# Kernel optimization log

Hardware: AMD Instinct MI355X
Metric: run time of the kernel (lower is better)

## Reference

```python
import jax, jax.numpy as jnp
import numpy as np

N, E, HDIM, NG = 10000, 320000, 256, 20
BN_EPS = 1e-5


def setup_inputs() -> dict:
    key = jax.random.key(0)
    ks = jax.random.split(key, 12)
    inp = {
        "x": jax.random.normal(ks[0], (N, HDIM), dtype=jnp.float32),
        "rbf": jax.random.uniform(ks[1], (E, NG), dtype=jnp.float32),
        "ei": jax.random.randint(ks[2], (2, E), 0, N, dtype=jnp.int64),
        # filter_net: Linear(n_g, hdim) -> SiLU -> Linear(hdim, hdim)
        "Wf1": jax.random.normal(ks[3], (NG, HDIM), dtype=jnp.float32) / np.sqrt(NG),
        "bf1": jnp.zeros((HDIM,), dtype=jnp.float32),
        "Wf2": jax.random.normal(ks[4], (HDIM, HDIM), dtype=jnp.float32) / np.sqrt(HDIM),
        "bf2": jnp.zeros((HDIM,), dtype=jnp.float32),
        # node_update: Linear(hdim, hdim) -> SiLU -> Linear(hdim, hdim)
        "Wu1": jax.random.normal(ks[5], (HDIM, HDIM), dtype=jnp.float32) / np.sqrt(HDIM),
        "bu1": jnp.zeros((HDIM,), dtype=jnp.float32),
        "Wu2": jax.random.normal(ks[6], (HDIM, HDIM), dtype=jnp.float32) / np.sqrt(HDIM),
        "bu2": jnp.zeros((HDIM,), dtype=jnp.float32),
        # BatchNorm1d affine params
        "gamma": jnp.ones((HDIM,), dtype=jnp.float32),
        "beta": jnp.zeros((HDIM,), dtype=jnp.float32),
    }
    return inp


def reference(x, rbf, Wf1, bf1, Wf2, bf2, Wu1, bu1, Wu2, bu2, gamma, beta, ei):
    row, col = ei[0], ei[1]
    # filter_net(rbf): [E, hdim]
    filt = jax.nn.silu(rbf @ Wf1 + bf1) @ Wf2 + bf2
    # message = gather(x, col) * filter
    msg = x[col] * filt  # [E, hdim]
    # scatter_add aggregation over destination nodes
    agg = jax.ops.segment_sum(msg, row, num_segments=x.shape[0])  # [N, hdim]
    # node_update MLP
    h = jax.nn.silu(agg @ Wu1 + bu1) @ Wu2 + bu2  # [N, hdim]
    # BatchNorm1d (training mode: batch stats, biased variance)
    mean = jnp.mean(h, axis=0)
    var = jnp.mean(jnp.square(h - mean), axis=0)
    bn = gamma * (h - mean) * jax.lax.rsqrt(var + BN_EPS) + beta
    return x + bn
```

## Files before the change

kernel.cpp:

```cpp
#include <hip/hip_runtime.h>

#define N_NODES 10000
#define E_EDGES 320000
#define HDIM    256
#define NG      20
#define BN_EPS  1e-5f

typedef __attribute__((ext_vector_type(8))) short short8;
typedef __attribute__((ext_vector_type(4))) float f32x4;

__device__ __forceinline__ float silu_f(float v) { return v / (1.0f + __expf(-v)); }

__device__ __forceinline__ unsigned short f2bf(float f) {
    union { float f; unsigned int u; } v; v.f = f;
    unsigned int r = v.u + 0x7fffu + ((v.u >> 16) & 1u);
    return (unsigned short)(r >> 16);
}

__global__ __launch_bounds__(256) void prep_kernel(
    const float* __restrict__ Wf2, const float* __restrict__ Wu1,
    const float* __restrict__ Wu2,
    unsigned short* __restrict__ Pf2, unsigned short* __restrict__ Pu1,
    unsigned short* __restrict__ Pu2)
{
    const float* W = (blockIdx.y == 0) ? Wf2 : (blockIdx.y == 1) ? Wu1 : Wu2;
    unsigned short* P = (blockIdx.y == 0) ? Pf2 : (blockIdx.y == 1) ? Pu1 : Pu2;
    int tid   = blockIdx.x * 256 + threadIdx.x;
    int j     = tid & 7;
    int lane  = (tid >> 3) & 63;
    int ntile = (tid >> 9) & 15;
    int kstep = tid >> 13;
    int k = kstep * 32 + (lane >> 4) * 8 + j;
    int n = ntile * 16 + (lane & 15);
    P[tid] = f2bf(W[k * 256 + n]);
}

__global__ __launch_bounds__(256) void prep1_kernel(
    const float* __restrict__ Wf1, const float* __restrict__ bf1,
    unsigned short* __restrict__ P1)
{
    int tid = blockIdx.x * 256 + threadIdx.x;
    int j     = tid & 7;
    int lane  = (tid >> 3) & 63;
    int ntile = tid >> 9;
    int k = (lane >> 4) * 8 + j;
    int n = ntile * 16 + (lane & 15);
    float v = (k < NG) ? Wf1[k * 256 + n] : (k == NG ? bf1[n] : 0.0f);
    P1[tid] = f2bf(v);
}

__global__ __launch_bounds__(256) void hist_kernel(const int* __restrict__ ei_row,
                                                   int* __restrict__ cnt) {
    int e = blockIdx.x * 256 + threadIdx.x;
    atomicAdd(&cnt[ei_row[e]], 1);
}

__global__ __launch_bounds__(256) void scan_kernel(int* __restrict__ cnt) {
    __shared__ int tot[256];
    const int t = threadIdx.x;
    int loc[40];
    int s = 0;
    #pragma unroll
    for (int i = 0; i < 40; ++i) { loc[i] = cnt[t * 40 + i]; s += loc[i]; }
    tot[t] = s;
    __syncthreads();
    for (int off = 1; off < 256; off <<= 1) {
        int u = (t >= off) ? tot[t - off] : 0;
        __syncthreads();
        tot[t] += u;
        __syncthreads();
    }
    int pre = tot[t] - s;
    #pragma unroll
    for (int i = 0; i < 40; ++i) { int v = loc[i]; cnt[t * 40 + i] = pre; pre += v; }
}

__global__ __launch_bounds__(256) void fill_kernel(const int* __restrict__ ei_row,
                                                   int* __restrict__ cnt,
                                                   int* __restrict__ perm,
                                                   int* __restrict__ nodepos) {
    int e = blockIdx.x * 256 + threadIdx.x;
    int r = ei_row[e];
    int pos = atomicAdd(&cnt[r], 1);
    perm[pos] = e;
    nodepos[pos] = r;
}

#define SM_A1  0
#define SM_NID 5120
#define SM_COL 5376
#define SM_HID 5632
#define SM_TOT 38400

__global__ __launch_bounds__(256, 3) void edge_kernel(
    const float* __restrict__ rbf, const int* __restrict__ ei_col,
    const int* __restrict__ perm, const int* __restrict__ nodepos,
    const unsigned short* __restrict__ P1, const unsigned short* __restrict__ P2,
    const float* __restrict__ bf2, const float* __restrict__ x,
    float* __restrict__ agg)
{
    __shared__ char sm[SM_TOT];
    unsigned short* A1 = (unsigned short*)(sm + SM_A1);
    int* nid_s = (int*)(sm + SM_NID);
    int* col_s = (int*)(sm + SM_COL);

    const int t  = threadIdx.x;
    const int p0 = blockIdx.x * 64;
    const int l = t & 63, w = t >> 6;
    const int l15 = l & 15, l4 = l >> 4;

    if (t < 64) {
        nid_s[t] = nodepos[p0 + t];
        col_s[t] = ei_col[perm[p0 + t]];
    }
    {
        const int row = t >> 2, q = t & 3;
        const int e = perm[p0 + row];
        const float* rp = rbf + (size_t)e * NG + q * 5;
        #pragma unroll
        for (int i = 0; i < 5; ++i) A1[row * 40 + q * 5 + i] = f2bf(rp[i]);
        if (q == 3) {
            A1[row * 40 + 20] = 0x3F80;
            #pragma unroll
            for (int k = 21; k < 32; ++k) A1[row * 40 + k] = 0;
        }
    }

    short8 b1[4];
    #pragma unroll
    for (int n = 0; n < 4; ++n)
        b1[n] = *(const short8*)(P1 + ((4 * w + n) * 64 + l) * 8);

    __syncthreads();

    f32x4 acc[4][4];
    #pragma unroll
    for (int n = 0; n < 4; ++n)
        #pragma unroll
        for (int m = 0; m < 4; ++m) acc[n][m] = (f32x4)0.0f;

    #pragma unroll
    for (int m = 0; m < 4; ++m) {
        short8 af = *(const short8*)(sm + SM_A1 + (m * 16 + l15) * 80 + l4 * 16);
        #pragma unroll
        for (int n = 0; n < 4; ++n)
            acc[n][m] = __builtin_amdgcn_mfma_f32_16x16x32_bf16(af, b1[n], acc[n][m], 0, 0, 0);
    }

    #pragma unroll
    for (int n = 0; n < 4; ++n) {
        const int col = w * 64 + n * 16 + l15;
        #pragma unroll
        for (int m = 0; m < 4; ++m)
            #pragma unroll
            for (int r = 0; r < 4; ++r) {
                int row = m * 16 + l4 * 4 + r;
                *(unsigned short*)(sm + SM_HID + row * 512 +
                    ((((col >> 3) ^ (row & 7))) << 4) + (col & 7) * 2) =
                    f2bf(silu_f(acc[n][m][r]));
            }
    }
    __syncthreads();

    #pragma unroll
    for (int n = 0; n < 4; ++n)
        #pragma unroll
        for (int m = 0; m < 4; ++m) acc[n][m] = (f32x4)0.0f;

    short8 bcur[4];
    #pragma unroll
    for (int n = 0; n < 4; ++n)
        bcur[n] = *(const short8*)(P2 + (((0 * 16 + 4 * w + n) * 64) + l) * 8);

    for (int ks = 0; ks < 8; ++ks) {
        short8 bnext[4];
        if (ks < 7) {
            #pragma unroll
            for (int n = 0; n < 4; ++n)
                bnext[n] = *(const short8*)(P2 + ((((ks + 1) * 16 + 4 * w + n) * 64) + l) * 8);
        }
        #pragma unroll
        for (int m = 0; m < 4; ++m) {
            const int row = m * 16 + l15;
            short8 af = *(const short8*)(sm + SM_HID + row * 512 +
                           ((((ks << 2) + l4) ^ (row & 7)) << 4));
            #pragma unroll
            for (int n = 0; n < 4; ++n)
                acc[n][m] = __builtin_amdgcn_mfma_f32_16x16x32_bf16(af, bcur[n], acc[n][m], 0, 0, 0);
        }
        if (ks < 7) {
            #pragma unroll
            for (int n = 0; n < 4; ++n) bcur[n] = bnext[n];
        }
    }
    __syncthreads();

    float bc[4];
    #pragma unroll
    for (int n = 0; n < 4; ++n) bc[n] = bf2[w * 64 + n * 16 + l15];

    float sum = 0.0f;
    int cur = nid_s[0];
    float* msgf = (float*)(sm + SM_HID);

    #pragma unroll
    for (int ms = 0; ms < 2; ++ms) {
        #pragma unroll
        for (int mm = 0; mm < 2; ++mm) {
            const int m = ms * 2 + mm;
            #pragma unroll
            for (int r = 0; r < 4; ++r) {
                const int row = m * 16 + l4 * 4 + r;
                const int pos = row & 31;
                const float* xp = x + (size_t)col_s[row] * HDIM;
                #pragma unroll
                for (int n = 0; n < 4; ++n) {
                    const int col = w * 64 + n * 16 + l15;
                    float mv = (acc[n][m][r] + bc[n]) * xp[col];
                    *(float*)(sm + SM_HID + pos * 1024 +
                        ((((col >> 2) ^ (pos & 7))) << 4) + (col & 3) * 4) = mv;
                }
            }
        }
        __syncthreads();
        for (int pos = 0; pos < 32; ++pos) {
            const int row = ms * 32 + pos;
            const int nid = nid_s[row];
            float v = *(const float*)(sm + SM_HID + pos * 1024 +
                        ((((t >> 2) ^ (pos & 7))) << 4) + (t & 3) * 4);
            if (nid != cur) {
                atomicAdd(&agg[(size_t)cur * HDIM + t], sum);
                sum = 0.0f; cur = nid;
            }
            sum += v;
        }
        __syncthreads();
    }
    atomicAdd(&agg[(size_t)cur * HDIM + t], sum);
}

__global__ __launch_bounds__(256, 3) void node_kernel(
    const float* __restrict__ agg, const float* __restrict__ bu1,
    const float* __restrict__ bu2,
    const unsigned short* __restrict__ Pu1, const unsigned short* __restrict__ Pu2,
    float* __restrict__ hout, float* __restrict__ sums)
{
    __shared__ unsigned short A[64 * 256];
    const int t  = threadIdx.x;
    const int r0 = blockIdx.x * 64;
    const int l = t & 63, w = t >> 6;
    const int l15 = l & 15, l4 = l >> 4;

    {
        const int kq = t >> 3, klo = t & 7;
        for (int row = 0; row < 64; ++row) {
            int gr = r0 + row;
            float v = (gr < N_NODES) ? agg[(size_t)gr * HDIM + t] : 0.0f;
            A[row * 256 + ((kq ^ (row & 7)) << 3) + klo] = f2bf(v);
        }
    }
    __syncthreads();

    f32x4 acc[4][4];
    #pragma unroll
    for (int n = 0; n < 4; ++n)
        #pragma unroll
        for (int m = 0; m < 4; ++m) acc[n][m] = (f32x4)0.0f;

    short8 bcur[4];
    #pragma unroll
    for (int n = 0; n < 4; ++n)
        bcur[n] = *(const short8*)(Pu1 + (((4 * w + n) * 64) + l) * 8);

    for (int ks = 0; ks < 8; ++ks) {
        short8 bnext[4];
        if (ks < 7) {
            #pragma unroll
            for (int n = 0; n < 4; ++n)
                bnext[n] = *(const short8*)(Pu1 + ((((ks + 1) * 16 + 4 * w + n) * 64) + l) * 8);
        }
        #pragma unroll
        for (int m = 0; m < 4; ++m) {
            const int row = m * 16 + l15;
            short8 af = *(const short8*)((char*)A + row * 512 +
                           ((((ks << 2) + l4) ^ (row & 7)) << 4));
            #pragma unroll
            for (int n = 0; n < 4; ++n)
                acc[n][m] = __builtin_amdgcn_mfma_f32_16x16x32_bf16(af, bcur[n], acc[n][m], 0, 0, 0);
        }
        if (ks < 7) {
            #pragma unroll
            for (int n = 0; n < 4; ++n) bcur[n] = bnext[n];
        }
    }
    __syncthreads();

    #pragma unroll
    for (int n = 0; n < 4; ++n) {
        const int col = w * 64 + n * 16 + l15;
        const float b = bu1[col];
        #pragma unroll
        for (int m = 0; m < 4; ++m)
            #pragma unroll
            for (int r = 0; r < 4; ++r) {
                int row = m * 16 + l4 * 4 + r;
                A[row * 256 + (((col >> 3) ^ (row & 7)) << 3) + (col & 7)] =
                    f2bf(silu_f(acc[n][m][r] + b));
            }
    }
    #pragma unroll
    for (int n = 0; n < 4; ++n)
        #pragma unroll
        for (int m = 0; m < 4; ++m) acc[n][m] = (f32x4)0.0f;
    __syncthreads();

    #pragma unroll
    for (int n = 0; n < 4; ++n)
        bcur[n] = *(const short8*)(Pu2 + (((4 * w + n) * 64) + l) * 8);

    for (int ks = 0; ks < 8; ++ks) {
        short8 bnext[4];
        if (ks < 7) {
            #pragma unroll
            for (int n = 0; n < 4; ++n)
                bnext[n] = *(const short8*)(Pu2 + ((((ks + 1) * 16 + 4 * w + n) * 64) + l) * 8);
        }
        #pragma unroll
        for (int m = 0; m < 4; ++m) {
            const int row = m * 16 + l15;
            short8 af = *(const short8*)((char*)A + row * 512 +
                           ((((ks << 2) + l4) ^ (row & 7)) << 4));
            #pragma unroll
            for (int n = 0; n < 4; ++n)
                acc[n][m] = __builtin_amdgcn_mfma_f32_16x16x32_bf16(af, bcur[n], acc[n][m], 0, 0, 0);
        }
        if (ks < 7) {
            #pragma unroll
            for (int n = 0; n < 4; ++n) bcur[n] = bnext[n];
        }
    }

    #pragma unroll
    for (int n = 0; n < 4; ++n) {
        const int col = w * 64 + n * 16 + l15;
        const float b = bu2[col];
        float s = 0.0f, s2 = 0.0f;
        #pragma unroll
        for (int m = 0; m < 4; ++m)
            #pragma unroll
            for (int r = 0; r < 4; ++r) {
                int gr = r0 + m * 16 + l4 * 4 + r;
                float h = acc[n][m][r] + b;
                if (gr < N_NODES) {
                    hout[(size_t)gr * HDIM + col] = h;
                    s += h; s2 += h * h;
                }
            }
        s  += __shfl_xor(s, 16);  s  += __shfl_xor(s, 32);
        s2 += __shfl_xor(s2, 16); s2 += __shfl_xor(s2, 32);
        if (l4 == 0) {
            atomicAdd(&sums[col], s);
            atomicAdd(&sums[HDIM + col], s2);
        }
    }
}

__global__ __launch_bounds__(256) void final_kernel(
    const float* __restrict__ x, const float* __restrict__ sums,
    const float* __restrict__ gamma, const float* __restrict__ beta,
    float* __restrict__ out)
{
    const int i = blockIdx.x * 256 + threadIdx.x;
    const int j = i & (HDIM - 1);
    const float mean = sums[j] * (1.0f / N_NODES);
    const float var  = sums[HDIM + j] * (1.0f / N_NODES) - mean * mean;
    const float inv  = rsqrtf(var + BN_EPS);
    const float hv   = out[i];
    out[i] = x[i] + gamma[j] * (hv - mean) * inv + beta[j];
}

extern "C" void kernel_launch(void* const* d_in, const int* in_sizes, int n_in,
                              void* d_out, int out_size, void* d_ws, size_t ws_size,
                              hipStream_t stream) {
    const float* x     = (const float*)d_in[0];
    const float* rbf   = (const float*)d_in[1];
    const int*   ei    = (const int*)d_in[2];
    const float* Wf1   = (const float*)d_in[3];
    const float* bf1   = (const float*)d_in[4];
    const float* Wf2   = (const float*)d_in[5];
    const float* bf2   = (const float*)d_in[6];
    const float* Wu1   = (const float*)d_in[7];
    const float* bu1   = (const float*)d_in[8];
    const float* Wu2   = (const float*)d_in[9];
    const float* bu2   = (const float*)d_in[10];
    const float* gamma = (const float*)d_in[11];
    const float* beta  = (const float*)d_in[12];
    float* out = (float*)d_out;

    char* ws = (char*)d_ws;
    float* agg     = (float*)(ws);
    float* sums    = (float*)(ws + 10240000);
    int*   cnt     = (int*)(ws + 10242048);
    int*   perm    = (int*)(ws + 10283008);
    int*   nodepos = (int*)(ws + 11563008);
    unsigned short* Pf2 = (unsigned short*)(ws + 12843008);
    unsigned short* Pu1 = (unsigned short*)(ws + 12974080);
    unsigned short* Pu2 = (unsigned short*)(ws + 13105152);
    unsigned short* P1  = (unsigned short*)(ws + 13236224);

    hipMemsetAsync(agg,  0, 10240000, stream);
    hipMemsetAsync(sums, 0, 2048, stream);
    hipMemsetAsync(cnt,  0, 40960, stream);

    prep_kernel<<<dim3(256, 3), 256, 0, stream>>>(Wf2, Wu1, Wu2, Pf2, Pu1, Pu2);
    prep1_kernel<<<32, 256, 0, stream>>>(Wf1, bf1, P1);
    hist_kernel<<<E_EDGES / 256, 256, 0, stream>>>(ei, cnt);
    scan_kernel<<<1, 256, 0, stream>>>(cnt);
    fill_kernel<<<E_EDGES / 256, 256, 0, stream>>>(ei, cnt, perm, nodepos);

    edge_kernel<<<E_EDGES / 64, 256, 0, stream>>>(
        rbf, ei + E_EDGES, perm, nodepos, P1, Pf2, bf2, x, agg);
    node_kernel<<<(N_NODES + 63) / 64, 256, 0, stream>>>(
        agg, bu1, bu2, Pu1, Pu2, out, sums);
    final_kernel<<<(N_NODES * HDIM) / 256, 256, 0, stream>>>(x, sums, gamma, beta, out);
}
```

Measured before the change: 219.7 us.

## Transpose MFMA operand roles, vectorize epilogues, merge prep kernels and memsets

Swaps the MFMA operand roles so weights are the A operand and activations the B operand. Each lane then holds four consecutive output columns, which allows packed bf16 conversion and vectorized float4 loads and stores of x, bias, hout and the staged messages. It also merges the Wf1 prep into the main prep kernel, merges three memsets into one, vectorizes the rbf and agg staging loads, swizzles the edge block order across groups of eight, and uses a hardware reciprocal in SiLU. Together these cut launch count, scalar memory ops and conversion instructions. The cost is a more intricate fragment mapping and slightly less precise SiLU.

```diff
diff --git a/kernel.cpp b/kernel.cpp
--- a/kernel.cpp
+++ b/kernel.cpp
@@ -9,7 +9,16 @@
 typedef __attribute__((ext_vector_type(8))) short short8;
 typedef __attribute__((ext_vector_type(4))) float f32x4;
 
-__device__ __forceinline__ float silu_f(float v) { return v / (1.0f + __expf(-v)); }
+__device__ __forceinline__ float silu_f(float v) {
+    float e = __expf(-v);
+    return v * __builtin_amdgcn_rcpf(1.0f + e);
+}
+
+__device__ __forceinline__ unsigned int cvt_pk(float lo, float hi) {
+    unsigned int r;
+    asm("v_cvt_pk_bf16_f32 %0, %1, %2" : "=v"(r) : "v"(lo), "v"(hi));
+    return r;
+}
 
 __device__ __forceinline__ unsigned short f2bf(float f) {
     union { float f; unsigned int u; } v; v.f = f;
@@ -19,10 +28,23 @@
 
 __global__ __launch_bounds__(256) void prep_kernel(
     const float* __restrict__ Wf2, const float* __restrict__ Wu1,
-    const float* __restrict__ Wu2,
+    const float* __restrict__ Wu2, const float* __restrict__ Wf1,
+    const float* __restrict__ bf1,
     unsigned short* __restrict__ Pf2, unsigned short* __restrict__ Pu1,
-    unsigned short* __restrict__ Pu2)
+    unsigned short* __restrict__ Pu2, unsigned short* __restrict__ P1)
 {
+    if (blockIdx.y == 3) {
+        if (blockIdx.x >= 32) return;
+        int tid = blockIdx.x * 256 + threadIdx.x;
+        int j     = tid & 7;
+        int lane  = (tid >> 3) & 63;
+        int ntile = tid >> 9;
+        int k = (lane >> 4) * 8 + j;
+        int n = ntile * 16 + (lane & 15);
+        float v = (k < NG) ? Wf1[k * 256 + n] : (k == NG ? bf1[n] : 0.0f);
+        P1[tid] = f2bf(v);
+        return;
+    }
     const float* W = (blockIdx.y == 0) ? Wf2 : (blockIdx.y == 1) ? Wu1 : Wu2;
     unsigned short* P = (blockIdx.y == 0) ? Pf2 : (blockIdx.y == 1) ? Pu1 : Pu2;
     int tid   = blockIdx.x * 256 + threadIdx.x;
@@ -35,20 +57,6 @@
     P[tid] = f2bf(W[k * 256 + n]);
 }
 
-__global__ __launch_bounds__(256) void prep1_kernel(
-    const float* __restrict__ Wf1, const float* __restrict__ bf1,
-    unsigned short* __restrict__ P1)
-{
-    int tid = blockIdx.x * 256 + threadIdx.x;
-    int j     = tid & 7;
-    int lane  = (tid >> 3) & 63;
-    int ntile = tid >> 9;
-    int k = (lane >> 4) * 8 + j;
-    int n = ntile * 16 + (lane & 15);
-    float v = (k < NG) ? Wf1[k * 256 + n] : (k == NG ? bf1[n] : 0.0f);
-    P1[tid] = f2bf(v);
-}
-
 __global__ __launch_bounds__(256) void hist_kernel(const int* __restrict__ ei_row,
                                                    int* __restrict__ cnt) {
     int e = blockIdx.x * 256 + threadIdx.x;
@@ -86,11 +94,11 @@
     nodepos[pos] = r;
 }
 
-#define SM_A1  0
-#define SM_NID 5120
-#define SM_COL 5376
-#define SM_HID 5632
-#define SM_TOT 38400
+#define SM_NID 0
+#define SM_COL 256
+#define SM_RBF 512
+#define SM_HID 4608
+#define SM_TOT 37376
 
 __global__ __launch_bounds__(256, 3) void edge_kernel(
     const float* __restrict__ rbf, const int* __restrict__ ei_col,
@@ -100,12 +108,13 @@
     float* __restrict__ agg)
 {
     __shared__ char sm[SM_TOT];
-    unsigned short* A1 = (unsigned short*)(sm + SM_A1);
     int* nid_s = (int*)(sm + SM_NID);
     int* col_s = (int*)(sm + SM_COL);
 
-    const int t  = threadIdx.x;
-    const int p0 = blockIdx.x * 64;
+    const int t = threadIdx.x;
+    int blk = blockIdx.x;
+    blk = (blk & 7) * (E_EDGES / 64 / 8) + (blk >> 3);
+    const int p0 = blk * 64;
     const int l = t & 63, w = t >> 6;
     const int l15 = l & 15, l4 = l >> 4;
 
@@ -113,113 +122,122 @@
         nid_s[t] = nodepos[p0 + t];
         col_s[t] = ei_col[perm[p0 + t]];
     }
-    {
-        const int row = t >> 2, q = t & 3;
-        const int e = perm[p0 + row];
-        const float* rp = rbf + (size_t)e * NG + q * 5;
-        #pragma unroll
-        for (int i = 0; i < 5; ++i) A1[row * 40 + q * 5 + i] = f2bf(rp[i]);
-        if (q == 3) {
-            A1[row * 40 + 20] = 0x3F80;
-            #pragma unroll
-            for (int k = 21; k < 32; ++k) A1[row * 40 + k] = 0;
-        }
-    }
-
-    short8 b1[4];
-    #pragma unroll
-    for (int n = 0; n < 4; ++n)
-        b1[n] = *(const short8*)(P1 + ((4 * w + n) * 64 + l) * 8);
+    if (t < 128) {
+        const int row = t >> 1, half = t & 1;
+        const float* rp = rbf + (size_t)perm[p0 + row] * NG + half * 10;
+        float v[10];
+        if (half == 0) {
+            float4 a = *(const float4*)rp, b = *(const float4*)(rp + 4);
+            float2 c = *(const float2*)(rp + 8);
+            v[0]=a.x; v[1]=a.y; v[2]=a.z; v[3]=a.w; v[4]=b.x;
+            v[5]=b.y; v[6]=b.z; v[7]=b.w; v[8]=c.x; v[9]=c.y;
+        } else {
+            float2 a = *(const float2*)rp;
+            float4 b = *(const float4*)(rp + 2), c = *(const float4*)(rp + 6);
+            v[0]=a.x; v[1]=a.y; v[2]=b.x; v[3]=b.y; v[4]=b.z;
+            v[5]=b.w; v[6]=c.x; v[7]=c.y; v[8]=c.z; v[9]=c.w;
+        }
+        unsigned int* dst = (unsigned int*)(sm + SM_RBF + row * 64 + half * 20);
+        #pragma unroll
+        for (int i = 0; i < 5; ++i) dst[i] = cvt_pk(v[2*i], v[2*i+1]);
+    } else if (t < 192) {
+        const int row = t - 128;
+        *(unsigned long long*)(sm + SM_RBF + row * 64 + 40) = 0x3F80ull;
+        *(uint4*)(sm + SM_RBF + row * 64 + 48) = make_uint4(0, 0, 0, 0);
+    }
+
+    short8 a1[4], acur[4];
+    #pragma unroll
+    for (int mt = 0; mt < 4; ++mt) {
+        a1[mt]   = *(const short8*)(P1 + ((4 * w + mt) * 64 + l) * 8);
+        acur[mt] = *(const short8*)(P2 + ((4 * w + mt) * 64 + l) * 8);
+    }
 
     __syncthreads();
 
     f32x4 acc[4][4];
     #pragma unroll
-    for (int n = 0; n < 4; ++n)
-        #pragma unroll
-        for (int m = 0; m < 4; ++m) acc[n][m] = (f32x4)0.0f;
-
-    #pragma unroll
-    for (int m = 0; m < 4; ++m) {
-        short8 af = *(const short8*)(sm + SM_A1 + (m * 16 + l15) * 80 + l4 * 16);
-        #pragma unroll
-        for (int n = 0; n < 4; ++n)
-            acc[n][m] = __builtin_amdgcn_mfma_f32_16x16x32_bf16(af, b1[n], acc[n][m], 0, 0, 0);
-    }
-
-    #pragma unroll
-    for (int n = 0; n < 4; ++n) {
-        const int col = w * 64 + n * 16 + l15;
-        #pragma unroll
-        for (int m = 0; m < 4; ++m)
-            #pragma unroll
-            for (int r = 0; r < 4; ++r) {
-                int row = m * 16 + l4 * 4 + r;
-                *(unsigned short*)(sm + SM_HID + row * 512 +
-                    ((((col >> 3) ^ (row & 7))) << 4) + (col & 7) * 2) =
-                    f2bf(silu_f(acc[n][m][r]));
-            }
-    }
-    __syncthreads();
-
-    #pragma unroll
-    for (int n = 0; n < 4; ++n)
-        #pragma unroll
-        for (int m = 0; m < 4; ++m) acc[n][m] = (f32x4)0.0f;
-
-    short8 bcur[4];
-    #pragma unroll
-    for (int n = 0; n < 4; ++n)
-        bcur[n] = *(const short8*)(P2 + (((0 * 16 + 4 * w + n) * 64) + l) * 8);
+    for (int mt = 0; mt < 4; ++mt)
+        #pragma unroll
+        for (int nt = 0; nt < 4; ++nt) acc[mt][nt] = (f32x4)0.0f;
+
+    #pragma unroll
+    for (int nt = 0; nt < 4; ++nt) {
+        short8 bfr = *(const short8*)(sm + SM_RBF + (nt * 16 + l15) * 64 + l4 * 16);
+        #pragma unroll
+        for (int mt = 0; mt < 4; ++mt)
+            acc[mt][nt] = __builtin_amdgcn_mfma_f32_16x16x32_bf16(a1[mt], bfr, acc[mt][nt], 0, 0, 0);
+    }
+
+    #pragma unroll
+    for (int mt = 0; mt < 4; ++mt) {
+        const int hc0 = w * 64 + mt * 16 + l4 * 4;
+        #pragma unroll
+        for (int nt = 0; nt < 4; ++nt) {
+            const int row = nt * 16 + l15;
+            unsigned int pk0 = cvt_pk(silu_f(acc[mt][nt][0]), silu_f(acc[mt][nt][1]));
+            unsigned int pk1 = cvt_pk(silu_f(acc[mt][nt][2]), silu_f(acc[mt][nt][3]));
+            *(uint2*)(sm + SM_HID + row * 512 +
+                      (((hc0 >> 3) ^ (row & 7)) << 4) + (hc0 & 7) * 2) =
+                make_uint2(pk0, pk1);
+        }
+    }
+    __syncthreads();
+
+    #pragma unroll
+    for (int mt = 0; mt < 4; ++mt)
+        #pragma unroll
+        for (int nt = 0; nt < 4; ++nt) acc[mt][nt] = (f32x4)0.0f;
 
     for (int ks = 0; ks < 8; ++ks) {
-        short8 bnext[4];
-        if (ks < 7) {
-            #pragma unroll
-            for (int n = 0; n < 4; ++n)
-                bnext[n] = *(const short8*)(P2 + ((((ks + 1) * 16 + 4 * w + n) * 64) + l) * 8);
-        }
-        #pragma unroll
-        for (int m = 0; m < 4; ++m) {
-            const int row = m * 16 + l15;
-            short8 af = *(const short8*)(sm + SM_HID + row * 512 +
-                           ((((ks << 2) + l4) ^ (row & 7)) << 4));
-            #pragma unroll
-            for (int n = 0; n < 4; ++n)
-                acc[n][m] = __builtin_amdgcn_mfma_f32_16x16x32_bf16(af, bcur[n], acc[n][m], 0, 0, 0);
-        }
-        if (ks < 7) {
-            #pragma unroll
-            for (int n = 0; n < 4; ++n) bcur[n] = bnext[n];
-        }
-    }
-    __syncthreads();
-
-    float bc[4];
-    #pragma unroll
-    for (int n = 0; n < 4; ++n) bc[n] = bf2[w * 64 + n * 16 + l15];
+        short8 anext[4];
+        if (ks < 7) {
+            #pragma unroll
+            for (int mt = 0; mt < 4; ++mt)
+                anext[mt] = *(const short8*)(P2 + (((ks + 1) * 16 + 4 * w + mt) * 64 + l) * 8);
+        }
+        #pragma unroll
+        for (int nt = 0; nt < 4; ++nt) {
+            const int row = nt * 16 + l15;
+            short8 bfh = *(const short8*)(sm + SM_HID + row * 512 +
+                            ((((ks << 2) + l4) ^ (row & 7)) << 4));
+            #pragma unroll
+            for (int mt = 0; mt < 4; ++mt)
+                acc[mt][nt] = __builtin_amdgcn_mfma_f32_16x16x32_bf16(acur[mt], bfh, acc[mt][nt], 0, 0, 0);
+        }
+        if (ks < 7) {
+            #pragma unroll
+            for (int mt = 0; mt < 4; ++mt) acur[mt] = anext[mt];
+        }
+    }
+    __syncthreads();
+
+    f32x4 bc4[4];
+    #pragma unroll
+    for (int mt = 0; mt < 4; ++mt)
+        bc4[mt] = *(const f32x4*)(bf2 + w * 64 + mt * 16 + l4 * 4);
+
+    const float* xbase[4];
+    #pragma unroll
+    for (int nt = 0; nt < 4; ++nt)
+        xbase[nt] = x + (size_t)col_s[nt * 16 + l15] * HDIM;
 
     float sum = 0.0f;
     int cur = nid_s[0];
-    float* msgf = (float*)(sm + SM_HID);
 
     #pragma unroll
     for (int ms = 0; ms < 2; ++ms) {
         #pragma unroll
-        for (int mm = 0; mm < 2; ++mm) {
-            const int m = ms * 2 + mm;
-            #pragma unroll
-            for (int r = 0; r < 4; ++r) {
-                const int row = m * 16 + l4 * 4 + r;
-                const int pos = row & 31;
-                const float* xp = x + (size_t)col_s[row] * HDIM;
-                #pragma unroll
-                for (int n = 0; n < 4; ++n) {
-                    const int col = w * 64 + n * 16 + l15;
-                    float mv = (acc[n][m][r] + bc[n]) * xp[col];
-                    *(float*)(sm + SM_HID + pos * 1024 +
-                        ((((col >> 2) ^ (pos & 7))) << 4) + (col & 3) * 4) = mv;
-                }
+        for (int ni = 0; ni < 2; ++ni) {
+            const int nt  = ms * 2 + ni;
+            const int pos = ni * 16 + l15;
+            #pragma unroll
+            for (int mt = 0; mt < 4; ++mt) {
+                const int fc0 = w * 64 + mt * 16 + l4 * 4;
+                f32x4 xv = *(const f32x4*)(xbase[nt] + fc0);
+                f32x4 mv = (acc[mt][nt] + bc4[mt]) * xv;
+                *(f32x4*)(sm + SM_HID + pos * 1024 +
+                          (((fc0 >> 2) ^ (pos & 7)) << 4)) = mv;
             }
         }
         __syncthreads();
@@ -227,7 +245,7 @@
             const int row = ms * 32 + pos;
             const int nid = nid_s[row];
             float v = *(const float*)(sm + SM_HID + pos * 1024 +
-                        ((((t >> 2) ^ (pos & 7))) << 4) + (t & 3) * 4);
+                        (((t >> 2) ^ (pos & 7)) << 4) + (t & 3) * 4);
             if (nid != cur) {
                 atomicAdd(&agg[(size_t)cur * HDIM + t], sum);
                 sum = 0.0f; cur = nid;
@@ -245,122 +263,131 @@
     const unsigned short* __restrict__ Pu1, const unsigned short* __restrict__ Pu2,
     float* __restrict__ hout, float* __restrict__ sums)
 {
-    __shared__ unsigned short A[64 * 256];
+    __shared__ char sm[32768];
     const int t  = threadIdx.x;
     const int r0 = blockIdx.x * 64;
     const int l = t & 63, w = t >> 6;
     const int l15 = l & 15, l4 = l >> 4;
 
     {
-        const int kq = t >> 3, klo = t & 7;
-        for (int row = 0; row < 64; ++row) {
-            int gr = r0 + row;
-            float v = (gr < N_NODES) ? agg[(size_t)gr * HDIM + t] : 0.0f;
-            A[row * 256 + ((kq ^ (row & 7)) << 3) + klo] = f2bf(v);
-        }
-    }
+        const int row = t & 63, q = t >> 6;
+        const bool valid = (r0 + row) < N_NODES;
+        const float4* src = (const float4*)(agg + (size_t)(r0 + row) * HDIM) + q * 16;
+        #pragma unroll
+        for (int i = 0; i < 16; ++i) {
+            float4 v = valid ? src[i] : make_float4(0.f, 0.f, 0.f, 0.f);
+            const int c0 = q * 64 + i * 4;
+            *(uint2*)(sm + row * 512 + (((c0 >> 3) ^ (row & 7)) << 4) + (c0 & 7) * 2) =
+                make_uint2(cvt_pk(v.x, v.y), cvt_pk(v.z, v.w));
+        }
+    }
+
+    short8 acur[4];
+    #pragma unroll
+    for (int mt = 0; mt < 4; ++mt)
+        acur[mt] = *(const short8*)(Pu1 + ((4 * w + mt) * 64 + l) * 8);
+
     __syncthreads();
 
     f32x4 acc[4][4];
     #pragma unroll
-    for (int n = 0; n < 4; ++n)
-        #pragma unroll
-        for (int m = 0; m < 4; ++m) acc[n][m] = (f32x4)0.0f;
-
-    short8 bcur[4];
-    #pragma unroll
-    for (int n = 0; n < 4; ++n)
-        bcur[n] = *(const short8*)(Pu1 + (((4 * w + n) * 64) + l) * 8);
+    for (int mt = 0; mt < 4; ++mt)
+        #pragma unroll
+        for (int nt = 0; nt < 4; ++nt) acc[mt][nt] = (f32x4)0.0f;
 
     for (int ks = 0; ks < 8; ++ks) {
-        short8 bnext[4];
-        if (ks < 7) {
-            #pragma unroll
-            for (int n = 0; n < 4; ++n)
-                bnext[n] = *(const short8*)(Pu1 + ((((ks + 1) * 16 + 4 * w + n) * 64) + l) * 8);
-        }
-        #pragma unroll
-        for (int m = 0; m < 4; ++m) {
-            const int row = m * 16 + l15;
-            short8 af = *(const short8*)((char*)A + row * 512 +
-                           ((((ks << 2) + l4) ^ (row & 7)) << 4));
-            #pragma unroll
-            for (int n = 0; n < 4; ++n)
-                acc[n][m] = __builtin_amdgcn_mfma_f32_16x16x32_bf16(af, bcur[n], acc[n][m], 0, 0, 0);
-        }
-        if (ks < 7) {
-            #pragma unroll
-            for (int n = 0; n < 4; ++n) bcur[n] = bnext[n];
-        }
-    }
-    __syncthreads();
-
-    #pragma unroll
-    for (int n = 0; n < 4; ++n) {
-        const int col = w * 64 + n * 16 + l15;
-        const float b = bu1[col];
-        #pragma unroll
-        for (int m = 0; m < 4; ++m)
+        short8 anext[4];
+        if (ks < 7) {
+            #pragma unroll
+            for (int mt = 0; mt < 4; ++mt)
+                anext[mt] = *(const short8*)(Pu1 + (((ks + 1) * 16 + 4 * w + mt) * 64 + l) * 8);
+        }
+        #pragma unroll
+        for (int nt = 0; nt < 4; ++nt) {
+            const int row = nt * 16 + l15;
+            short8 bfa = *(const short8*)(sm + row * 512 +
+                            ((((ks << 2) + l4) ^ (row & 7)) << 4));
+            #pragma unroll
+            for (int mt = 0; mt < 4; ++mt)
+                acc[mt][nt] = __builtin_amdgcn_mfma_f32_16x16x32_bf16(acur[mt], bfa, acc[mt][nt], 0, 0, 0);
+        }
+        if (ks < 7) {
+            #pragma unroll
+            for (int mt = 0; mt < 4; ++mt) acur[mt] = anext[mt];
+        }
+    }
+    __syncthreads();
+
+    #pragma unroll
+    for (int mt = 0; mt < 4; ++mt)
+        acur[mt] = *(const short8*)(Pu2 + ((4 * w + mt) * 64 + l) * 8);
+
+    #pragma unroll
+    for (int mt = 0; mt < 4; ++mt) {
+        const int mc0 = w * 64 + mt * 16 + l4 * 4;
+        f32x4 b4 = *(const f32x4*)(bu1 + mc0);
+        #pragma unroll
+        for (int nt = 0; nt < 4; ++nt) {
+            const int row = nt * 16 + l15;
+            unsigned int pk0 = cvt_pk(silu_f(acc[mt][nt][0] + b4[0]), silu_f(acc[mt][nt][1] + b4[1]));
+            unsigned int pk1 = cvt_pk(silu_f(acc[mt][nt][2] + b4[2]), silu_f(acc[mt][nt][3] + b4[3]));
+            *(uint2*)(sm + row * 512 + (((mc0 >> 3) ^ (row & 7)) << 4) + (mc0 & 7) * 2) =
+                make_uint2(pk0, pk1);
+            acc[mt][nt] = (f32x4)0.0f;
+        }
+    }
+    __syncthreads();
+
+    for (int ks = 0; ks < 8; ++ks) {
+        short8 anext[4];
+        if (ks < 7) {
+            #pragma unroll
+            for (int mt = 0; mt < 4; ++mt)
+                anext[mt] = *(const short8*)(Pu2 + (((ks + 1) * 16 + 4 * w + mt) * 64 + l) * 8);
+        }
+        #pragma unroll
+        for (int nt = 0; nt < 4; ++nt) {
+            const int row = nt * 16 + l15;
+            short8 bfm = *(const short8*)(sm + row * 512 +
+                            ((((ks << 2) + l4) ^ (row & 7)) << 4));
+            #pragma unroll
+            for (int mt = 0; mt < 4; ++mt)
+                acc[mt][nt] = __builtin_amdgcn_mfma_f32_16x16x32_bf16(acur[mt], bfm, acc[mt][nt], 0, 0, 0);
+        }
+        if (ks < 7) {
+            #pragma unroll
+            for (int mt = 0; mt < 4; ++mt) acur[mt] = anext[mt];
+        }
+    }
+
+    #pragma unroll
+    for (int mt = 0; mt < 4; ++mt) {
+        const int hc0 = w * 64 + mt * 16 + l4 * 4;
+        f32x4 b4 = *(const f32x4*)(bu2 + hc0);
+        f32x4 s = (f32x4)0.0f, s2 = (f32x4)0.0f;
+        #pragma unroll
+        for (int nt = 0; nt < 4; ++nt) {
+            const int gr = r0 + nt * 16 + l15;
+            if (gr < N_NODES) {
+                f32x4 hv = acc[mt][nt] + b4;
+                *(f32x4*)(hout + (size_t)gr * HDIM + hc0) = hv;
+                s += hv; s2 += hv * hv;
+            }
+        }
+        #pragma unroll
+        for (int off = 1; off < 16; off <<= 1) {
             #pragma unroll
             for (int r = 0; r < 4; ++r) {
-                int row = m * 16 + l4 * 4 + r;
-                A[row * 256 + (((col >> 3) ^ (row & 7)) << 3) + (col & 7)] =
-                    f2bf(silu_f(acc[n][m][r] + b));
+                s[r]  += __shfl_xor(s[r], off);
+                s2[r] += __shfl_xor(s2[r], off);
             }
-    }
-    #pragma unroll
-    for (int n = 0; n < 4; ++n)
-        #pragma unroll
-        for (int m = 0; m < 4; ++m) acc[n][m] = (f32x4)0.0f;
-    __syncthreads();
-
-    #pragma unroll
-    for (int n = 0; n < 4; ++n)
-        bcur[n] = *(const short8*)(Pu2 + (((4 * w + n) * 64) + l) * 8);
-
-    for (int ks = 0; ks < 8; ++ks) {
-        short8 bnext[4];
-        if (ks < 7) {
-            #pragma unroll
-            for (int n = 0; n < 4; ++n)
-                bnext[n] = *(const short8*)(Pu2 + ((((ks + 1) * 16 + 4 * w + n) * 64) + l) * 8);
-        }
-        #pragma unroll
-        for (int m = 0; m < 4; ++m) {
-            const int row = m * 16 + l15;
-            short8 af = *(const short8*)((char*)A + row * 512 +
-                           ((((ks << 2) + l4) ^ (row & 7)) << 4));
-            #pragma unroll
-            for (int n = 0; n < 4; ++n)
-                acc[n][m] = __builtin_amdgcn_mfma_f32_16x16x32_bf16(af, bcur[n], acc[n][m], 0, 0, 0);
-        }
-        if (ks < 7) {
-            #pragma unroll
-            for (int n = 0; n < 4; ++n) bcur[n] = bnext[n];
-        }
-    }
-
-    #pragma unroll
-    for (int n = 0; n < 4; ++n) {
-        const int col = w * 64 + n * 16 + l15;
-        const float b = bu2[col];
-        float s = 0.0f, s2 = 0.0f;
-        #pragma unroll
-        for (int m = 0; m < 4; ++m)
+        }
+        if (l15 == 0) {
             #pragma unroll
             for (int r = 0; r < 4; ++r) {
-                int gr = r0 + m * 16 + l4 * 4 + r;
-                float h = acc[n][m][r] + b;
-                if (gr < N_NODES) {
-                    hout[(size_t)gr * HDIM + col] = h;
-                    s += h; s2 += h * h;
-                }
+                atomicAdd(&sums[hc0 + r], s[r]);
+                atomicAdd(&sums[HDIM + hc0 + r], s2[r]);
             }
-        s  += __shfl_xor(s, 16);  s  += __shfl_xor(s, 32);
-        s2 += __shfl_xor(s2, 16); s2 += __shfl_xor(s2, 32);
-        if (l4 == 0) {
-            atomicAdd(&sums[col], s);
-            atomicAdd(&sums[HDIM + col], s2);
         }
     }
 }
@@ -408,12 +435,10 @@
     unsigned short* Pu2 = (unsigned short*)(ws + 13105152);
     unsigned short* P1  = (unsigned short*)(ws + 13236224);
 
-    hipMemsetAsync(agg,  0, 10240000, stream);
-    hipMemsetAsync(sums, 0, 2048, stream);
-    hipMemsetAsync(cnt,  0, 40960, stream);
-
-    prep_kernel<<<dim3(256, 3), 256, 0, stream>>>(Wf2, Wu1, Wu2, Pf2, Pu1, Pu2);
-    prep1_kernel<<<32, 256, 0, stream>>>(Wf1, bf1, P1);
+    hipMemsetAsync(agg, 0, 10283008, stream);
+
+    prep_kernel<<<dim3(256, 4), 256, 0, stream>>>(Wf2, Wu1, Wu2, Wf1, bf1,
+                                                  Pf2, Pu1, Pu2, P1);
     hist_kernel<<<E_EDGES / 256, 256, 0, stream>>>(ei, cnt);
     scan_kernel<<<1, 256, 0, stream>>>(cnt);
     fill_kernel<<<E_EDGES / 256, 256, 0, stream>>>(ei, cnt, perm, nodepos);
```

Result: faster. 205.5 us (-6.5%).
